# Kernel optimization log

Hardware: AMD Instinct MI355X
Metric: run time of the kernel (lower is better)

Reference implementation:

```python
import jax, jax.numpy as jnp
import numpy as np

IN_DIM = 2048


def setup_inputs() -> dict:
    key = jax.random.key(0)
    ks = jax.random.split(key, 7)
    s = 1.0 / np.sqrt(IN_DIM)
    x = jax.random.normal(ks[0], (8, 256, IN_DIM), dtype=jnp.float32)
    Wq = jax.random.uniform(ks[1], (IN_DIM, IN_DIM), jnp.float32, -s, s)
    bq = jax.random.uniform(ks[2], (IN_DIM,), jnp.float32, -s, s)
    Wk = jax.random.uniform(ks[3], (IN_DIM, IN_DIM), jnp.float32, -s, s)
    bk = jax.random.uniform(ks[4], (IN_DIM,), jnp.float32, -s, s)
    Wv = jax.random.uniform(ks[5], (IN_DIM, IN_DIM), jnp.float32, -s, s)
    bv = jax.random.uniform(ks[6], (IN_DIM,), jnp.float32, -s, s)
    return {"x": x, "Wq": Wq, "bq": bq, "Wk": Wk, "bk": bk, "Wv": Wv, "bv": bv}


def reference(x, Wq, bq, Wk, bk, Wv, bv):
    # x: [B, C, L]; Linear acts on last (L) axis; torch Linear: y = x @ W^T + b
    scale = 1.0 / jnp.sqrt(jnp.asarray(x.shape[-1], x.dtype))
    q = jnp.einsum('bcl,ml->bcm', x, Wq) + bq
    k = jnp.einsum('bcl,ml->bcm', x, Wk) + bk
    v = jnp.einsum('bcl,ml->bcm', x, Wv) + bv
    # attn[b,l,m] = sum_c q[b,c,l] * k[b,c,m]
    attn = jnp.einsum('bcl,bcm->blm', q, k) * scale  # [B, L, L]
    attn = jax.nn.softmax(attn, axis=-1)
    # out[b,c,l] = sum_m v[b,c,m] * attn[b,l,m]
    out = jnp.einsum('bcm,blm->bcl', v, attn)  # [B, C, L]
    return out
```

## Files before the change

### kernel.cpp

```cpp
#include <hip/hip_runtime.h>
#include <hip/hip_bf16.h>
#include <cstdint>
#include <cstddef>


typedef __bf16 bf16_t;
typedef _Float16 fp16_t;
typedef __bf16 bf16x8 __attribute__((ext_vector_type(8)));
typedef __bf16 bf16x4 __attribute__((ext_vector_type(4)));
typedef float floatx4 __attribute__((ext_vector_type(4)));

#define GLD_LDS16(gptr, lptr)                                                  \
  __builtin_amdgcn_global_load_lds(                                            \
      (const __attribute__((address_space(1))) void*)(gptr),                   \
      (__attribute__((address_space(3))) void*)(lptr), 16, 0, 0)

__global__ __launch_bounds__(256) void cvt4_f32_bf16(
    const float* __restrict__ s0, const float* __restrict__ s1,
    const float* __restrict__ s2, const float* __restrict__ s3,
    bf16_t* __restrict__ d0, bf16_t* __restrict__ d1,
    bf16_t* __restrict__ d2, bf16_t* __restrict__ d3) {
  const float* s;
  bf16_t* d;
  switch (blockIdx.y) {
    case 0: s = s0; d = d0; break;
    case 1: s = s1; d = d1; break;
    case 2: s = s2; d = d2; break;
    default: s = s3; d = d3; break;
  }
  const int i = (blockIdx.x * 256 + threadIdx.x) * 4;
  const float4 v = *reinterpret_cast<const float4*>(s + i);
  bf16x4 o;
  o[0] = (bf16_t)v.x; o[1] = (bf16_t)v.y; o[2] = (bf16_t)v.z; o[3] = (bf16_t)v.w;
  *reinterpret_cast<bf16x4*>(d + i) = o;
}

__global__ __launch_bounds__(256) void gemm_qkv(
    const bf16_t* __restrict__ xb, const bf16_t* __restrict__ Wball,
    bf16_t* __restrict__ tT, bf16_t* __restrict__ vb,
    const float* __restrict__ bq, const float* __restrict__ bk,
    const float* __restrict__ bv) {
  __shared__ __align__(16) bf16_t lds_a[128 * 32];
  __shared__ __align__(16) bf16_t lds_b[128 * 32];

  constexpr long M4 = 4l * 1024 * 1024;
  const int tid = threadIdx.x;
  const int lane = tid & 63;
  const int wid = tid >> 6;
  const int brow = blockIdx.x * 128;
  const int bcol = blockIdx.y * 128;
  const int wr = wid >> 1, wc = wid & 1;
  const int z = blockIdx.z;

  const bf16_t* A = xb;
  const bf16_t* B = Wball + (long)z * M4;

  floatx4 acc[4][4];
#pragma unroll
  for (int m = 0; m < 4; m++)
#pragma unroll
    for (int n = 0; n < 4; n++) acc[m][n] = (floatx4)0.f;

  const int c0 = wid * 2, c1 = wid * 2 + 1;
  const int srow0 = c0 * 16 + (lane >> 2);
  const int srow1 = c1 * 16 + (lane >> 2);
  const int skoff = (lane & 3) * 8;

  for (int kk = 0; kk < 2048; kk += 32) {
    GLD_LDS16(A + (size_t)(brow + srow0) * 2048 + kk + skoff, lds_a + c0 * 512);
    GLD_LDS16(A + (size_t)(brow + srow1) * 2048 + kk + skoff, lds_a + c1 * 512);
    GLD_LDS16(B + (size_t)(bcol + srow0) * 2048 + kk + skoff, lds_b + c0 * 512);
    GLD_LDS16(B + (size_t)(bcol + srow1) * 2048 + kk + skoff, lds_b + c1 * 512);
    __syncthreads();

    bf16x8 af[4], bfr[4];
#pragma unroll
    for (int m = 0; m < 4; m++)
      af[m] = *(const bf16x8*)&lds_a[(wr * 64 + m * 16 + (lane & 15)) * 32 +
                                     (lane >> 4) * 8];
#pragma unroll
    for (int n = 0; n < 4; n++)
      bfr[n] = *(const bf16x8*)&lds_b[(wc * 64 + n * 16 + (lane & 15)) * 32 +
                                      (lane >> 4) * 8];
#pragma unroll
    for (int m = 0; m < 4; m++)
#pragma unroll
      for (int n = 0; n < 4; n++)
        acc[m][n] =
            __builtin_amdgcn_mfma_f32_16x16x32_bf16(af[m], bfr[n], acc[m][n], 0, 0, 0);
    __syncthreads();
  }

  const int r0 = (lane >> 4) * 4;
  const int cc = lane & 15;
  const float* bias = (z == 0) ? bq : (z == 1) ? bk : bv;

  if (z < 2) {
    bf16_t* C = tT + (long)z * M4;
#pragma unroll
    for (int n = 0; n < 4; n++) {
      const int gj = bcol + wc * 64 + n * 16 + cc;
      const float badd = bias[gj];
#pragma unroll
      for (int m = 0; m < 4; m++) {
        const int gi = brow + wr * 64 + m * 16 + r0;
        bf16x4 o;
#pragma unroll
        for (int r = 0; r < 4; r++) o[r] = (bf16_t)(acc[m][n][r] + badd);
        *(bf16x4*)&C[(size_t)gj * 2048 + gi] = o;
      }
    }
  } else {
    bf16_t* C = vb;
#pragma unroll
    for (int n = 0; n < 4; n++) {
      const int gj = bcol + wc * 64 + n * 16 + cc;
      const float badd = bias[gj];
#pragma unroll
      for (int m = 0; m < 4; m++) {
        const int gi = brow + wr * 64 + m * 16 + r0;
#pragma unroll
        for (int r = 0; r < 4; r++)
          C[(size_t)(gi + r) * 2048 + gj] = (bf16_t)(acc[m][n][r] + badd);
      }
    }
  }
}

__global__ __launch_bounds__(256, 2) void flash3(
    const bf16_t* __restrict__ qT, const bf16_t* __restrict__ kT,
    const bf16_t* __restrict__ v, fp16_t* __restrict__ po,
    float* __restrict__ pl) {
  __shared__ __align__(16) bf16_t Ks[8192];
  __shared__ __align__(16) bf16_t Vs[8192];
  __shared__ __align__(16) bf16_t Ps[4 * 1280];

  const int tid = threadIdx.x, lane = tid & 63, w = tid >> 6;
  const int idx = blockIdx.x;
  const int b = idx & 7, sg = (idx >> 3) & 3, qt = idx >> 5;
  const int l0 = qt * 128;
  const int key0 = sg * 512;
  const int i15 = lane & 15, g4 = lane >> 4;

  const bf16_t* Qg = qT + (size_t)(l0 + w * 32) * 2048 + b * 256;
  const bf16_t* Kg = kT + (size_t)key0 * 2048 + b * 256;
  const bf16_t* Vg = v + (size_t)b * 256 * 2048 + key0;

  bf16x8 af0[8], af1[8];
#pragma unroll
  for (int ks = 0; ks < 8; ks++) {
    af0[ks] = *(const bf16x8*)&Qg[(size_t)i15 * 2048 + ks * 32 + g4 * 8];
    af1[ks] = *(const bf16x8*)&Qg[(size_t)(16 + i15) * 2048 + ks * 32 + g4 * 8];
  }

  const int srow = lane >> 2;
  const int sslot = (lane & 3) ^ ((lane >> 3) & 3);
  auto stageK = [&](const bf16_t* g) {
#pragma unroll
    for (int j = 0; j < 4; j++) {
      const int ch = w * 4 + j, ks = ch >> 1, mseg = ch & 1;
      GLD_LDS16(g + (size_t)(mseg * 16 + srow) * 2048 + ks * 32 + sslot * 8,
                Ks + ch * 512);
    }
  };
  auto stageV = [&](const bf16_t* g) {
#pragma unroll
    for (int j = 0; j < 4; j++) {
      const int ch = w * 4 + j;
      GLD_LDS16(g + (size_t)(ch * 16 + srow) * 2048 + sslot * 8, Vs + ch * 512);
    }
  };

  floatx4 acc_o0[16], acc_o1[16];
#pragma unroll
  for (int cf = 0; cf < 16; cf++) {
    acc_o0[cf] = (floatx4)0.f;
    acc_o1[cf] = (floatx4)0.f;
  }
  floatx4 acc_l0 = (floatx4)0.f, acc_l1 = (floatx4)0.f;

  bf16x8 vones;
#pragma unroll
  for (int j = 0; j < 8; j++) vones[j] = (bf16_t)1.0f;

  const float SC = 0.031880107f;
  const int slotr = g4 ^ ((i15 >> 1) & 3);

  stageK(Kg);
  stageV(Vg);
  __syncthreads();

  for (int t = 0; t < 16; t++) {
    floatx4 s00 = (floatx4)0.f, s01 = (floatx4)0.f;
    floatx4 s10 = (floatx4)0.f, s11 = (floatx4)0.f;
#pragma unroll
    for (int ks = 0; ks < 8; ks++) {
      const bf16x8 b0 = *(const bf16x8*)&Ks[ks * 1024 + i15 * 32 + slotr * 8];
      const bf16x8 b1 =
          *(const bf16x8*)&Ks[ks * 1024 + (16 + i15) * 32 + slotr * 8];
      s00 = __builtin_amdgcn_mfma_f32_16x16x32_bf16(af0[ks], b0, s00, 0, 0, 0);
      s01 = __builtin_amdgcn_mfma_f32_16x16x32_bf16(af0[ks], b1, s01, 0, 0, 0);
      s10 = __builtin_amdgcn_mfma_f32_16x16x32_bf16(af1[ks], b0, s10, 0, 0, 0);
      s11 = __builtin_amdgcn_mfma_f32_16x16x32_bf16(af1[ks], b1, s11, 0, 0, 0);
    }
    __syncthreads();
    if (t < 15) stageK(Kg + (size_t)(t + 1) * 32 * 2048);

    bf16_t* Pw = Ps + w * 1280;
#pragma unroll
    for (int r = 0; r < 4; r++) {
      Pw[(g4 * 4 + r) * 40 + i15] = (bf16_t)exp2f(s00[r] * SC);
      Pw[(g4 * 4 + r) * 40 + 16 + i15] = (bf16_t)exp2f(s01[r] * SC);
      Pw[(16 + g4 * 4 + r) * 40 + i15] = (bf16_t)exp2f(s10[r] * SC);
      Pw[(16 + g4 * 4 + r) * 40 + 16 + i15] = (bf16_t)exp2f(s11[r] * SC);
    }
    const bf16x8 pa0 = *(const bf16x8*)&Pw[i15 * 40 + g4 * 8];
    const bf16x8 pa1 = *(const bf16x8*)&Pw[(16 + i15) * 40 + g4 * 8];
    acc_l0 = __builtin_amdgcn_mfma_f32_16x16x32_bf16(pa0, vones, acc_l0, 0, 0, 0);
    acc_l1 = __builtin_amdgcn_mfma_f32_16x16x32_bf16(pa1, vones, acc_l1, 0, 0, 0);
#pragma unroll
    for (int cf = 0; cf < 16; cf++) {
      const bf16x8 bv = *(const bf16x8*)&Vs[(cf * 16 + i15) * 32 + slotr * 8];
      acc_o0[cf] = __builtin_amdgcn_mfma_f32_16x16x32_bf16(pa0, bv, acc_o0[cf], 0, 0, 0);
      acc_o1[cf] = __builtin_amdgcn_mfma_f32_16x16x32_bf16(pa1, bv, acc_o1[cf], 0, 0, 0);
    }
    __syncthreads();
    if (t < 15) stageV(Vg + (t + 1) * 32);
  }

  fp16_t* pob = po + ((size_t)(b * 4 + sg) * 2048 + l0 + w * 32) * 256;
#pragma unroll
  for (int cf = 0; cf < 16; cf++)
#pragma unroll
    for (int r = 0; r < 4; r++) {
      pob[(size_t)(g4 * 4 + r) * 256 + cf * 16 + i15] = (fp16_t)acc_o0[cf][r];
      pob[(size_t)(16 + g4 * 4 + r) * 256 + cf * 16 + i15] =
          (fp16_t)acc_o1[cf][r];
    }
  if (i15 == 0) {
    float* plb = pl + (size_t)(b * 4 + sg) * 2048 + l0 + w * 32;
#pragma unroll
    for (int r = 0; r < 4; r++) {
      plb[g4 * 4 + r] = acc_l0[r];
      plb[16 + g4 * 4 + r] = acc_l1[r];
    }
  }
}

__global__ __launch_bounds__(256) void combine4(
    const fp16_t* __restrict__ po, const float* __restrict__ pl,
    float* __restrict__ out) {
  __shared__ float invd[32];
  __shared__ float tile[32][33];
  const int lt = blockIdx.x, ct = blockIdx.y, b = blockIdx.z;
  const int l0 = lt * 32, c0 = ct * 32;
  const int t = threadIdx.x;

  if (t < 32) {
    float d = 0.f;
#pragma unroll
    for (int s = 0; s < 4; s++) d += pl[(size_t)(b * 4 + s) * 2048 + l0 + t];
    invd[t] = 1.f / d;
  }
  __syncthreads();

  const int c = t & 31;
#pragma unroll
  for (int pass = 0; pass < 4; pass++) {
    const int l = pass * 8 + (t >> 5);
    float acc = 0.f;
#pragma unroll
    for (int s = 0; s < 4; s++)
      acc += (float)po[((size_t)(b * 4 + s) * 2048 + l0 + l) * 256 + c0 + c];
    tile[c][l] = acc * invd[l];
  }
  __syncthreads();

  const int oc = t >> 3, lw = (t & 7) * 4;
  float4 val = {tile[oc][lw], tile[oc][lw + 1], tile[oc][lw + 2], tile[oc][lw + 3]};
  *(float4*)&out[((size_t)b * 256 + c0 + oc) * 2048 + l0 + lw] = val;
}

extern "C" void kernel_launch(void* const* d_in, const int* in_sizes, int n_in,
                              void* d_out, int out_size, void* d_ws,
                              size_t ws_size, hipStream_t stream) {
  const float* x = (const float*)d_in[0];
  float* out = (float*)d_out;

  constexpr long M4 = 4l * 1024 * 1024;
  bf16_t* ws = (bf16_t*)d_ws;
  bf16_t* xb = ws;
  bf16_t* Wb = ws + M4;
  bf16_t* tT = ws + 4 * M4;
  bf16_t* vb = ws + 6 * M4;
  fp16_t* po = (fp16_t*)(ws + 7 * M4);
  float* pl = (float*)(po + 8l * 4 * 2048 * 256);

  cvt4_f32_bf16<<<dim3(4096, 4), 256, 0, stream>>>(
      x, (const float*)d_in[1], (const float*)d_in[3], (const float*)d_in[5],
      xb, Wb, Wb + M4, Wb + 2 * M4);

  gemm_qkv<<<dim3(16, 16, 3), 256, 0, stream>>>(
      xb, Wb, tT, vb, (const float*)d_in[2], (const float*)d_in[4],
      (const float*)d_in[6]);

  flash3<<<dim3(512), 256, 0, stream>>>(tT, tT + M4, vb, po, pl);

  combine4<<<dim3(64, 8, 8), 256, 0, stream>>>(po, pl, out);
}
```

Measured before the change: 228.2 us.

## Rewrite QKV GEMM as 256x256-tile double-buffered pipelined kernel with 8 waves

```diff
diff --git a/kernel.cpp b/kernel.cpp
--- a/kernel.cpp
+++ b/kernel.cpp
@@ -14,6 +14,14 @@
   __builtin_amdgcn_global_load_lds(                                            \
       (const __attribute__((address_space(1))) void*)(gptr),                   \
       (__attribute__((address_space(3))) void*)(lptr), 16, 0, 0)
+
+#define BARRAW()                                                               \
+  do {                                                                         \
+    __builtin_amdgcn_sched_barrier(0);                                         \
+    asm volatile("" ::: "memory");                                             \
+    __builtin_amdgcn_s_barrier();                                              \
+    __builtin_amdgcn_sched_barrier(0);                                         \
+  } while (0)
 
 __global__ __launch_bounds__(256) void cvt4_f32_bf16(
     const float* __restrict__ s0, const float* __restrict__ s1,
@@ -35,93 +43,129 @@
   *reinterpret_cast<bf16x4*>(d + i) = o;
 }
 
-__global__ __launch_bounds__(256) void gemm_qkv(
-    const bf16_t* __restrict__ xb, const bf16_t* __restrict__ Wball,
+__global__ __launch_bounds__(512, 2) void gemm_qkv8(
+    const bf16_t* __restrict__ xb, const bf16_t* __restrict__ Wp,
     bf16_t* __restrict__ tT, bf16_t* __restrict__ vb,
     const float* __restrict__ bq, const float* __restrict__ bk,
     const float* __restrict__ bv) {
-  __shared__ __align__(16) bf16_t lds_a[128 * 32];
-  __shared__ __align__(16) bf16_t lds_b[128 * 32];
+  __shared__ __align__(16) bf16_t As[2 * 16384];
+  __shared__ __align__(16) bf16_t Bs[2 * 16384];
 
   constexpr long M4 = 4l * 1024 * 1024;
-  const int tid = threadIdx.x;
-  const int lane = tid & 63;
-  const int wid = tid >> 6;
-  const int brow = blockIdx.x * 128;
-  const int bcol = blockIdx.y * 128;
-  const int wr = wid >> 1, wc = wid & 1;
-  const int z = blockIdx.z;
-
-  const bf16_t* A = xb;
-  const bf16_t* B = Wball + (long)z * M4;
-
-  floatx4 acc[4][4];
-#pragma unroll
-  for (int m = 0; m < 4; m++)
+  const int tid = threadIdx.x, lane = tid & 63, w = tid >> 6;
+  const int i15 = lane & 15, g4 = lane >> 4;
+  const int wm = w >> 2, wn = w & 3;
+
+  const int o = blockIdx.x;
+  const int swz = (o & 7) * 24 + (o >> 3);
+  const int mx = swz & 7, nx = swz >> 3;
+  const int brow = mx * 256, bcol = nx * 256;
+
+  const int srow = tid >> 2, sslot = tid & 3;
+  const bf16_t* Ag = xb + (size_t)(brow + srow) * 2048 + sslot * 8;
+  const bf16_t* Bg = Wp + (size_t)(bcol + srow) * 2048 + sslot * 8;
+
+  auto stage_ht = [&](int h) {
+    const int tile = h >> 2, buf = tile & 1, part = h & 3;
+    const int kk = part >> 1;
+    const bool isA = part & 1;
+    const bf16_t* g = (isA ? Ag : Bg) + tile * 64 + kk * 32;
+    bf16_t* l = (isA ? As : Bs) + buf * 16384 + kk * 8192 + w * 512;
+    GLD_LDS16(g, l);
+    GLD_LDS16(g + (size_t)128 * 2048, l + 4096);
+  };
+
+  floatx4 acc[8][4];
+#pragma unroll
+  for (int m = 0; m < 8; m++)
 #pragma unroll
     for (int n = 0; n < 4; n++) acc[m][n] = (floatx4)0.f;
 
-  const int c0 = wid * 2, c1 = wid * 2 + 1;
-  const int srow0 = c0 * 16 + (lane >> 2);
-  const int srow1 = c1 * 16 + (lane >> 2);
-  const int skoff = (lane & 3) * 8;
-
-  for (int kk = 0; kk < 2048; kk += 32) {
-    GLD_LDS16(A + (size_t)(brow + srow0) * 2048 + kk + skoff, lds_a + c0 * 512);
-    GLD_LDS16(A + (size_t)(brow + srow1) * 2048 + kk + skoff, lds_a + c1 * 512);
-    GLD_LDS16(B + (size_t)(bcol + srow0) * 2048 + kk + skoff, lds_b + c0 * 512);
-    GLD_LDS16(B + (size_t)(bcol + srow1) * 2048 + kk + skoff, lds_b + c1 * 512);
-    __syncthreads();
-
-    bf16x8 af[4], bfr[4];
-#pragma unroll
-    for (int m = 0; m < 4; m++)
-      af[m] = *(const bf16x8*)&lds_a[(wr * 64 + m * 16 + (lane & 15)) * 32 +
-                                     (lane >> 4) * 8];
-#pragma unroll
-    for (int n = 0; n < 4; n++)
-      bfr[n] = *(const bf16x8*)&lds_b[(wc * 64 + n * 16 + (lane & 15)) * 32 +
-                                      (lane >> 4) * 8];
-#pragma unroll
-    for (int m = 0; m < 4; m++)
-#pragma unroll
-      for (int n = 0; n < 4; n++)
-        acc[m][n] =
-            __builtin_amdgcn_mfma_f32_16x16x32_bf16(af[m], bfr[n], acc[m][n], 0, 0, 0);
-    __syncthreads();
-  }
-
-  const int r0 = (lane >> 4) * 4;
-  const int cc = lane & 15;
-  const float* bias = (z == 0) ? bq : (z == 1) ? bk : bv;
-
-  if (z < 2) {
-    bf16_t* C = tT + (long)z * M4;
-#pragma unroll
-    for (int n = 0; n < 4; n++) {
-      const int gj = bcol + wc * 64 + n * 16 + cc;
-      const float badd = bias[gj];
-#pragma unroll
-      for (int m = 0; m < 4; m++) {
-        const int gi = brow + wr * 64 + m * 16 + r0;
-        bf16x4 o;
-#pragma unroll
-        for (int r = 0; r < 4; r++) o[r] = (bf16_t)(acc[m][n][r] + badd);
-        *(bf16x4*)&C[(size_t)gj * 2048 + gi] = o;
-      }
-    }
-  } else {
-    bf16_t* C = vb;
-#pragma unroll
-    for (int n = 0; n < 4; n++) {
-      const int gj = bcol + wc * 64 + n * 16 + cc;
-      const float badd = bias[gj];
-#pragma unroll
-      for (int m = 0; m < 4; m++) {
-        const int gi = brow + wr * 64 + m * 16 + r0;
+  bf16x8 Ar[4], Br[4];
+
+#define LDA(buf, kk, mh)                                                       \
+  {                                                                            \
+    const bf16_t* ab = As + (buf) * 16384 + (kk) * 8192 +                      \
+                       (wm * 128 + (mh) * 64 + i15) * 32 + g4 * 8;             \
+    Ar[0] = *(const bf16x8*)&ab[0 * 512];                                      \
+    Ar[1] = *(const bf16x8*)&ab[1 * 512];                                      \
+    Ar[2] = *(const bf16x8*)&ab[2 * 512];                                      \
+    Ar[3] = *(const bf16x8*)&ab[3 * 512];                                      \
+  }
+#define LDB(buf, kk)                                                           \
+  {                                                                            \
+    const bf16_t* bb = Bs + (buf) * 16384 + (kk) * 8192 +                      \
+                       (wn * 64 + i15) * 32 + g4 * 8;                          \
+    Br[0] = *(const bf16x8*)&bb[0 * 512];                                      \
+    Br[1] = *(const bf16x8*)&bb[1 * 512];                                      \
+    Br[2] = *(const bf16x8*)&bb[2 * 512];                                      \
+    Br[3] = *(const bf16x8*)&bb[3 * 512];                                      \
+  }
+#define MMA(mh)                                                                \
+  {                                                                            \
+    __builtin_amdgcn_s_setprio(1);                                             \
+    _Pragma("unroll") for (int mf = 0; mf < 4; mf++)                           \
+        _Pragma("unroll") for (int nf = 0; nf < 4; nf++)                       \
+        acc[(mh) * 4 + mf][nf] = __builtin_amdgcn_mfma_f32_16x16x32_bf16(      \
+            Ar[mf], Br[nf], acc[(mh) * 4 + mf][nf], 0, 0, 0);                  \
+    __builtin_amdgcn_s_setprio(0);                                             \
+  }
+
+  for (int h = 0; h < 7; ++h) stage_ht(h);
+  asm volatile("s_waitcnt vmcnt(6)" ::: "memory");
+  BARRAW();
+
+  for (int j = 0; j < 16; ++j) {
+    const int hb = 8 * j + 6;
+    LDB(0, 0); LDA(0, 0, 0);
+    stage_ht(hb + 1); BARRAW(); MMA(0); BARRAW();
+    LDA(0, 0, 1);
+    if (hb + 2 < 128) stage_ht(hb + 2); BARRAW(); MMA(1); BARRAW();
+    LDB(0, 1); LDA(0, 1, 0);
+    if (hb + 3 < 128) stage_ht(hb + 3); BARRAW(); MMA(0);
+    BARRAW();
+    LDA(0, 1, 1);
+    if (hb + 4 < 128) stage_ht(hb + 4); BARRAW(); MMA(1);
+    __builtin_amdgcn_sched_barrier(0);
+    if (j == 15)
+      asm volatile("s_waitcnt vmcnt(0)" ::: "memory");
+    else
+      asm volatile("s_waitcnt vmcnt(6)" ::: "memory");
+    BARRAW();
+    LDB(1, 0); LDA(1, 0, 0);
+    if (hb + 5 < 128) stage_ht(hb + 5); BARRAW(); MMA(0); BARRAW();
+    LDA(1, 0, 1);
+    if (hb + 6 < 128) stage_ht(hb + 6); BARRAW(); MMA(1); BARRAW();
+    LDB(1, 1); LDA(1, 1, 0);
+    if (hb + 7 < 128) stage_ht(hb + 7); BARRAW(); MMA(0); BARRAW();
+    LDA(1, 1, 1);
+    if (hb + 8 < 128) stage_ht(hb + 8); BARRAW(); MMA(1);
+    __builtin_amdgcn_sched_barrier(0);
+    if (j < 15) asm volatile("s_waitcnt vmcnt(6)" ::: "memory");
+    BARRAW();
+  }
+#undef LDA
+#undef LDB
+#undef MMA
+
+#pragma unroll
+  for (int nf = 0; nf < 4; nf++) {
+    const int gj = bcol + wn * 64 + nf * 16 + i15;
+    const int z = gj >> 11, jj = gj & 2047;
+    const float* bp = (z == 0) ? bq : (z == 1) ? bk : bv;
+    const float badd = bp[jj];
+#pragma unroll
+    for (int mf = 0; mf < 8; mf++) {
+      const int gi = brow + wm * 128 + mf * 16 + g4 * 4;
+      if (z < 2) {
+        bf16x4 ov;
+#pragma unroll
+        for (int r = 0; r < 4; r++) ov[r] = (bf16_t)(acc[mf][nf][r] + badd);
+        *(bf16x4*)&tT[(size_t)z * M4 + (size_t)jj * 2048 + gi] = ov;
+      } else {
 #pragma unroll
         for (int r = 0; r < 4; r++)
-          C[(size_t)(gi + r) * 2048 + gj] = (bf16_t)(acc[m][n][r] + badd);
+          vb[(size_t)(gi + r) * 2048 + jj] = (bf16_t)(acc[mf][nf][r] + badd);
       }
     }
   }
@@ -300,7 +344,7 @@
       x, (const float*)d_in[1], (const float*)d_in[3], (const float*)d_in[5],
       xb, Wb, Wb + M4, Wb + 2 * M4);
 
-  gemm_qkv<<<dim3(16, 16, 3), 256, 0, stream>>>(
+  gemm_qkv8<<<dim3(192), 512, 0, stream>>>(
       xb, Wb, tT, vb, (const float*)d_in[2], (const float*)d_in[4],
       (const float*)d_in[6]);
 
```

New measurement: 234.1 us. 2.6% more time.
